# Optimization experiments

Measured on AMD Instinct MI355X. Metric: run time of the kernel, lower is better.

Reference implementation:

```python
import jax, jax.numpy as jnp
import numpy as np

B = 65536
N_WORKER, N_PROJECT, EMB = 1807, 2490, 10
STATE_DIM = 2 * EMB          # 20
HIDDEN = 2 * STATE_DIM       # 40
ACTION_DIM = EMB             # 10


def setup_inputs() -> dict:
    key = jax.random.key(0)
    ks = jax.random.split(key, 8)
    worker_ids = jax.random.randint(ks[0], (B,), 0, N_WORKER)
    project_ids = jax.random.randint(ks[1], (B,), 0, N_PROJECT)
    worker_emb = jax.random.normal(ks[2], (N_WORKER, EMB), dtype=jnp.float32)
    project_emb = jax.random.normal(ks[3], (N_PROJECT, EMB), dtype=jnp.float32)
    W1 = jax.random.normal(ks[4], (HIDDEN, STATE_DIM), dtype=jnp.float32) / np.sqrt(STATE_DIM)
    b1 = jnp.zeros((HIDDEN,), dtype=jnp.float32)
    W2 = jax.random.normal(ks[5], (ACTION_DIM, HIDDEN), dtype=jnp.float32) / np.sqrt(HIDDEN)
    b2 = jnp.zeros((ACTION_DIM,), dtype=jnp.float32)
    return {"worker_ids": worker_ids, "project_ids": project_ids,
            "worker_emb": worker_emb, "project_emb": project_emb,
            "W1": W1, "b1": b1, "W2": W2, "b2": b2}


def reference(worker_ids, project_ids, worker_emb, project_emb, W1, b1, W2, b2):
    we = worker_emb[worker_ids]              # [B, 10]
    pe = project_emb[project_ids]            # [B, 10]
    x = jnp.concatenate([we, pe], axis=-1)   # [B, 20]
    h = jax.nn.relu(x @ W1.T + b1)           # [B, 40]
    the_weights = (h @ W2.T + b2)[:, None, :]  # [B, 1, 10]
    # original loop rebuilds rows 1..2489 of the project table -> single slice
    table = project_emb[1:N_PROJECT]         # [2489, 10]
    p = jnp.einsum('bqd,nd->bqn', the_weights, table)  # [B, 1, 2489]
    argmax = jnp.argmax(p, axis=2)           # [B, 1]
    return argmax + 1
```

## Files before the change

### kernel.cpp

```cpp
#include <hip/hip_runtime.h>
#include <float.h>

using v2f = __attribute__((ext_vector_type(2))) float;
using v4f = __attribute__((ext_vector_type(4))) float;

#define EMB 10
#define STATE 20
#define HIDDEN 40
#define NPROJ 2490
#define WAVES 16
#define ITEMS 128

__device__ __forceinline__ void score_pair2(const v4f* __restrict__ tp, int p,
                                            const v2f wv[2][5],
                                            float best[2], int bidx[2]) {
    v4f a0 = tp[0], a1 = tp[1], a2 = tp[2], a3 = tp[3], a4 = tp[4];
    #pragma unroll
    for (int g = 0; g < 2; ++g) {
        v2f c0 = wv[g][0] * a0.lo;
        c0 += wv[g][1] * a0.hi; c0 += wv[g][2] * a1.lo;
        c0 += wv[g][3] * a1.hi; c0 += wv[g][4] * a2.lo;
        float s0 = c0.x + c0.y;
        v2f c1 = wv[g][0] * a2.hi;
        c1 += wv[g][1] * a3.lo; c1 += wv[g][2] * a3.hi;
        c1 += wv[g][3] * a4.lo; c1 += wv[g][4] * a4.hi;
        float s1 = c1.x + c1.y;
        float sp = s0; int ip = 2 * p;
        if (s1 > sp) { sp = s1; ip = 2 * p + 1; }
        if (sp > best[g]) { best[g] = sp; bidx[g] = ip; }
    }
}

__global__ __launch_bounds__(1024, 8) void actor_kernel(
    const int* __restrict__ wid, const int* __restrict__ pid,
    const float* __restrict__ wemb, const float* __restrict__ pemb,
    const float* __restrict__ W1, const float* __restrict__ b1,
    const float* __restrict__ W2, const float* __restrict__ b2,
    int* __restrict__ out)
{
    __shared__ v2f   sw[ITEMS][5];
    __shared__ float sb[WAVES][ITEMS];
    __shared__ int   si[WAVES][ITEMS];

    const int tid  = threadIdx.x;
    const int lane = tid & 63;
    const int wave = tid >> 6;
    const int itemBase = blockIdx.x * ITEMS;

    const v4f* __restrict__ tbl4 =
        (const v4f*)__builtin_assume_aligned(pemb, 16);

    if (wave < ITEMS / 64) {
        const int b = itemBase + wave * 64 + lane;
        const int wi = wid[b];
        const int pi = pid[b];
        const float* __restrict__ wr = wemb + wi * EMB;
        const float* __restrict__ pr = pemb + pi * EMB;
        v2f x2[STATE / 2];
        #pragma unroll
        for (int k = 0; k < EMB / 2; ++k) x2[k] = *(const v2f*)(wr + 2 * k);
        #pragma unroll
        for (int k = 0; k < EMB / 2; ++k) x2[EMB / 2 + k] = *(const v2f*)(pr + 2 * k);

        float hb[HIDDEN];
        #pragma unroll 4
        for (int j = 0; j < HIDDEN; ++j) {
            const v2f* w1r = (const v2f*)(W1 + j * STATE);
            v2f a = w1r[0] * x2[0];
            #pragma unroll
            for (int k = 1; k < STATE / 2; ++k) a += w1r[k] * x2[k];
            hb[j] = fmaxf(a.x + a.y + b1[j], 0.0f);
        }
        v2f h2[HIDDEN / 2];
        #pragma unroll
        for (int k = 0; k < HIDDEN / 2; ++k) h2[k] = (v2f){hb[2 * k], hb[2 * k + 1]};

        #pragma unroll
        for (int d = 0; d < EMB; d += 2) {
            const v2f* w2r0 = (const v2f*)(W2 + d * HIDDEN);
            const v2f* w2r1 = (const v2f*)(W2 + (d + 1) * HIDDEN);
            v2f a0 = w2r0[0] * h2[0];
            v2f a1 = w2r1[0] * h2[0];
            #pragma unroll
            for (int k = 1; k < HIDDEN / 2; ++k) { a0 += w2r0[k] * h2[k]; a1 += w2r1[k] * h2[k]; }
            sw[wave * 64 + lane][d / 2] = (v2f){a0.x + a0.y + b2[d], a1.x + a1.y + b2[d + 1]};
        }
    }
    __syncthreads();

    v2f wv[2][5];
    #pragma unroll
    for (int g = 0; g < 2; ++g) {
        #pragma unroll
        for (int k = 0; k < 5; ++k) wv[g][k] = sw[g * 64 + lane][k];
    }

    float best[2];
    int   bidx[2];
    #pragma unroll
    for (int g = 0; g < 2; ++g) { best[g] = -FLT_MAX; bidx[g] = 1; }

    if (wave == 0) {
        v2f c0v = *(const v2f*)(pemb + 10);
        v4f c1v = *(const v4f*)(pemb + 12);
        v4f c2v = *(const v4f*)(pemb + 16);
        #pragma unroll
        for (int g = 0; g < 2; ++g) {
            v2f a = wv[g][0] * c0v;
            a += wv[g][1] * c1v.lo; a += wv[g][2] * c1v.hi;
            a += wv[g][3] * c2v.lo; a += wv[g][4] * c2v.hi;
            best[g] = a.x + a.y; bidx[g] = 1;
        }
    }

    int start = (wave < 12) ? (1 + 78 * wave) : (937 + 77 * (wave - 12));
    int cnt   = (wave < 12) ? 78 : 77;
    start = __builtin_amdgcn_readfirstlane(start);
    cnt   = __builtin_amdgcn_readfirstlane(cnt);

    const v4f* tp = tbl4 + start * 5;
    #pragma unroll 4
    for (int i = 0; i < cnt; ++i, tp += 5)
        score_pair2(tp, start + i, wv, best, bidx);

    #pragma unroll
    for (int g = 0; g < 2; ++g) {
        sb[wave][g * 64 + lane] = best[g];
        si[wave][g * 64 + lane] = bidx[g];
    }
    __syncthreads();

    if (tid < ITEMS) {
        float bb = sb[0][tid];
        int   bi = si[0][tid];
        #pragma unroll
        for (int w = 1; w < WAVES; ++w) {
            float v  = sb[w][tid];
            int   vi = si[w][tid];
            if (v > bb) { bb = v; bi = vi; }
        }
        out[itemBase + tid] = bi;
    }
}

extern "C" void kernel_launch(void* const* d_in, const int* in_sizes, int n_in,
                              void* d_out, int out_size, void* d_ws, size_t ws_size,
                              hipStream_t stream) {
    const int*   wid  = (const int*)  d_in[0];
    const int*   pid  = (const int*)  d_in[1];
    const float* wemb = (const float*)d_in[2];
    const float* pemb = (const float*)d_in[3];
    const float* W1   = (const float*)d_in[4];
    const float* b1   = (const float*)d_in[5];
    const float* W2   = (const float*)d_in[6];
    const float* b2   = (const float*)d_in[7];
    int* out = (int*)d_out;

    const int B = in_sizes[0];
    actor_kernel<<<B / ITEMS, 1024, 0, stream>>>(wid, pid, wemb, pemb, W1, b1, W2, b2, out);
}
```

Baseline: 128.6 us.

## Split MLP into separate kernel and scan with compile-time ranges

Moves the per-item MLP into its own kernel that writes action vectors to workspace. A second kernel loads those vectors and scans the project table, with each wave's range fixed at compile time through a template switch. This keeps the MLP's register pressure and the 2-of-16-wave idle phase out of the scan kernel and lets the scan loops be fully specialized. The cost is an extra launch plus a workspace round trip of B*10 floats, and it falls back to the fused kernel if no workspace is available.

```diff
diff --git a/kernel.cpp b/kernel.cpp
--- a/kernel.cpp
+++ b/kernel.cpp
@@ -10,6 +10,51 @@
 #define NPROJ 2490
 #define WAVES 16
 #define ITEMS 128
+
+__global__ __launch_bounds__(256, 4) void mlp_kernel(
+    const int* __restrict__ wid, const int* __restrict__ pid,
+    const float* __restrict__ wemb, const float* __restrict__ pemb,
+    const float* __restrict__ W1, const float* __restrict__ b1,
+    const float* __restrict__ W2, const float* __restrict__ b2,
+    float* __restrict__ ws)
+{
+    const int b = blockIdx.x * 256 + threadIdx.x;
+
+    const int wi = wid[b];
+    const int pi = pid[b];
+    const float* __restrict__ wr = wemb + wi * EMB;
+    const float* __restrict__ pr = pemb + pi * EMB;
+    v2f x2[STATE / 2];
+    #pragma unroll
+    for (int k = 0; k < EMB / 2; ++k) x2[k] = *(const v2f*)(wr + 2 * k);
+    #pragma unroll
+    for (int k = 0; k < EMB / 2; ++k) x2[EMB / 2 + k] = *(const v2f*)(pr + 2 * k);
+
+    float hb[HIDDEN];
+    #pragma unroll 4
+    for (int j = 0; j < HIDDEN; ++j) {
+        const v2f* w1r = (const v2f*)(W1 + j * STATE);
+        v2f a = w1r[0] * x2[0];
+        #pragma unroll
+        for (int k = 1; k < STATE / 2; ++k) a += w1r[k] * x2[k];
+        hb[j] = fmaxf(a.x + a.y + b1[j], 0.0f);
+    }
+    v2f h2[HIDDEN / 2];
+    #pragma unroll
+    for (int k = 0; k < HIDDEN / 2; ++k) h2[k] = (v2f){hb[2 * k], hb[2 * k + 1]};
+
+    v2f* wout = (v2f*)(ws + b * EMB);
+    #pragma unroll
+    for (int d = 0; d < EMB; d += 2) {
+        const v2f* w2r0 = (const v2f*)(W2 + d * HIDDEN);
+        const v2f* w2r1 = (const v2f*)(W2 + (d + 1) * HIDDEN);
+        v2f a0 = w2r0[0] * h2[0];
+        v2f a1 = w2r1[0] * h2[0];
+        #pragma unroll
+        for (int k = 1; k < HIDDEN / 2; ++k) { a0 += w2r0[k] * h2[k]; a1 += w2r1[k] * h2[k]; }
+        wout[d / 2] = (v2f){a0.x + a0.y + b2[d], a1.x + a1.y + b2[d + 1]};
+    }
+}
 
 __device__ __forceinline__ void score_pair2(const v4f* __restrict__ tp, int p,
                                             const v2f wv[2][5],
@@ -31,6 +76,101 @@
     }
 }
 
+template <int P0, int P1>
+__device__ __forceinline__ void scan_range(const v4f* __restrict__ tbl4,
+                                           const v2f wv[2][5],
+                                           float best[2], int bidx[2]) {
+    const v4f* tp = tbl4 + P0 * 5;
+    #pragma unroll 4
+    for (int p = P0; p < P1; ++p, tp += 5) score_pair2(tp, p, wv, best, bidx);
+}
+
+__global__ __launch_bounds__(1024, 8) void scan_kernel(
+    const float* __restrict__ pemb, const float* __restrict__ ws,
+    int* __restrict__ out)
+{
+    __shared__ float sb[WAVES][ITEMS];
+    __shared__ int   si[WAVES][ITEMS];
+
+    const int tid  = threadIdx.x;
+    const int lane = tid & 63;
+    const int wave = tid >> 6;
+    const int itemBase = blockIdx.x * ITEMS;
+
+    const v4f* __restrict__ tbl4 =
+        (const v4f*)__builtin_assume_aligned(pemb, 16);
+
+    v2f wv[2][5];
+    #pragma unroll
+    for (int g = 0; g < 2; ++g) {
+        const v2f* src = (const v2f*)(ws + (itemBase + g * 64 + lane) * EMB);
+        #pragma unroll
+        for (int k = 0; k < 5; ++k) wv[g][k] = src[k];
+    }
+
+    float best[2];
+    int   bidx[2];
+    #pragma unroll
+    for (int g = 0; g < 2; ++g) { best[g] = -FLT_MAX; bidx[g] = 1; }
+
+    if (wave == 0) {
+        v2f c0v = *(const v2f*)(pemb + 10);
+        v4f c1v = *(const v4f*)(pemb + 12);
+        v4f c2v = *(const v4f*)(pemb + 16);
+        #pragma unroll
+        for (int g = 0; g < 2; ++g) {
+            v2f a = wv[g][0] * c0v;
+            a += wv[g][1] * c1v.lo; a += wv[g][2] * c1v.hi;
+            a += wv[g][3] * c2v.lo; a += wv[g][4] * c2v.hi;
+            best[g] = a.x + a.y; bidx[g] = 1;
+        }
+    }
+
+    switch (wave) {
+        case  0: scan_range<   1,   79>(tbl4, wv, best, bidx); break;
+        case  1: scan_range<  79,  157>(tbl4, wv, best, bidx); break;
+        case  2: scan_range< 157,  235>(tbl4, wv, best, bidx); break;
+        case  3: scan_range< 235,  313>(tbl4, wv, best, bidx); break;
+        case  4: scan_range< 313,  391>(tbl4, wv, best, bidx); break;
+        case  5: scan_range< 391,  469>(tbl4, wv, best, bidx); break;
+        case  6: scan_range< 469,  547>(tbl4, wv, best, bidx); break;
+        case  7: scan_range< 547,  625>(tbl4, wv, best, bidx); break;
+        case  8: scan_range< 625,  703>(tbl4, wv, best, bidx); break;
+        case  9: scan_range< 703,  781>(tbl4, wv, best, bidx); break;
+        case 10: scan_range< 781,  859>(tbl4, wv, best, bidx); break;
+        case 11: scan_range< 859,  937>(tbl4, wv, best, bidx); break;
+        case 12: scan_range< 937, 1014>(tbl4, wv, best, bidx); break;
+        case 13: scan_range<1014, 1091>(tbl4, wv, best, bidx); break;
+        case 14: scan_range<1091, 1168>(tbl4, wv, best, bidx); break;
+        case 15: scan_range<1168, 1245>(tbl4, wv, best, bidx); break;
+    }
+
+    #pragma unroll
+    for (int g = 0; g < 2; ++g) {
+        sb[wave][g * 64 + lane] = best[g];
+        si[wave][g * 64 + lane] = bidx[g];
+    }
+    __syncthreads();
+
+    if (tid < ITEMS) {
+        float bb = sb[0][tid];
+        int   bi = si[0][tid];
+        #pragma unroll
+        for (int w = 1; w < WAVES; ++w) {
+            float v  = sb[w][tid];
+            int   vi = si[w][tid];
+            if (v > bb) { bb = v; bi = vi; }
+        }
+        out[itemBase + tid] = bi;
+    }
+}
+
+__device__ __forceinline__ void score_pair2_rt(const v4f* __restrict__ tp, int p,
+                                               const v2f wv[2][5],
+                                               float best[2], int bidx[2]) {
+    score_pair2(tp, p, wv, best, bidx);
+}
+
 __global__ __launch_bounds__(1024, 8) void actor_kernel(
     const int* __restrict__ wid, const int* __restrict__ pid,
     const float* __restrict__ wemb, const float* __restrict__ pemb,
@@ -121,7 +261,7 @@
     const v4f* tp = tbl4 + start * 5;
     #pragma unroll 4
     for (int i = 0; i < cnt; ++i, tp += 5)
-        score_pair2(tp, start + i, wv, best, bidx);
+        score_pair2_rt(tp, start + i, wv, best, bidx);
 
     #pragma unroll
     for (int g = 0; g < 2; ++g) {
@@ -157,5 +297,13 @@
     int* out = (int*)d_out;
 
     const int B = in_sizes[0];
-    actor_kernel<<<B / ITEMS, 1024, 0, stream>>>(wid, pid, wemb, pemb, W1, b1, W2, b2, out);
-}
+    const size_t ws_needed = (size_t)B * EMB * sizeof(float);
+
+    if (d_ws != nullptr && ws_size >= ws_needed) {
+        float* ws = (float*)d_ws;
+        mlp_kernel<<<B / 256, 256, 0, stream>>>(wid, pid, wemb, pemb, W1, b1, W2, b2, ws);
+        scan_kernel<<<B / ITEMS, 1024, 0, stream>>>(pemb, ws, out);
+    } else {
+        actor_kernel<<<B / ITEMS, 1024, 0, stream>>>(wid, pid, wemb, pemb, W1, b1, W2, b2, out);
+    }
+}
```

After: 131.4 us. +2.2%, slower.
